# Kernel tuning notes

Hardware: AMD Instinct MI355X
Metric: run time of the kernel (lower is better)

The kernel has to match this reference:

```python
import jax, jax.numpy as jnp
import numpy as np

B, H, S, D = 4, 16, 4096, 64

def setup_inputs() -> dict:
    key = jax.random.key(0)
    k1, k2, k3 = jax.random.split(key, 3)
    Q = jax.random.normal(k1, (B, H, S, D), dtype=jnp.float32)
    K = jax.random.normal(k2, (B, H, S, D), dtype=jnp.float32)
    V = jax.random.normal(k3, (B, H, S, D), dtype=jnp.float32)
    mask = jnp.ones((B, H, S), dtype=jnp.float32)
    return {"Q": Q, "K": K, "V": V, "mask": mask}

def reference(Q, K, V, mask):
    # elu(x)+1 feature map
    Qf = jax.nn.elu(Q) + 1.0
    Kf = (jax.nn.elu(K) + 1.0) * mask[..., None]
    # KV: [B,H,D,D] = sum_s K[s]^T V[s]
    KV = jnp.einsum('bhsd,bhse->bhde', Kf, V)
    # normalization: Z = 1 / (Q . sum_s K[s])  -> [B,H,S,1]
    Ksum = jnp.sum(Kf, axis=-2)  # [B,H,D]
    Z = 1.0 / jnp.einsum('bhsd,bhd->bhs', Qf, Ksum)[..., None]
    out = jnp.einsum('bhsd,bhde->bhse', Qf, KV) * Z
    return out
```

## Files before the change

### kernel.cpp

```cpp
#include <hip/hip_runtime.h>

#define S_LEN 4096
#define DIM 64
#define NHEAD 64
#define LDK 68
#define PHEAD 4160

__device__ __forceinline__ float elu1(float x) {
    return x > 0.0f ? x + 1.0f : __expf(x);
}

__global__ __launch_bounds__(256) void pass1_kv(
    const float* __restrict__ K, const float* __restrict__ V,
    const float* __restrict__ mask, float* __restrict__ partials, int sh)
{
    const int head  = blockIdx.x >> sh;
    const int chunk = blockIdx.x & ((1 << sh) - 1);
    const int ntile = (S_LEN / 64) >> sh;
    const int t  = threadIdx.x;
    const int tx = t & 15;
    const int ty = t >> 4;
    const int e0 = tx * 4;
    const int d0 = ty * 4;

    __shared__ float kf[64 * LDK];
    __shared__ float vf[64 * LDK];

    float acc[4][4] = {{0.f,0.f,0.f,0.f},{0.f,0.f,0.f,0.f},{0.f,0.f,0.f,0.f},{0.f,0.f,0.f,0.f}};
    float ks[4] = {0.f, 0.f, 0.f, 0.f};

    const long hbase = (long)head * S_LEN * DIM;

    for (int tile = 0; tile < ntile; ++tile) {
        const int sbase = (chunk * ntile + tile) * 64;
        __syncthreads();
        #pragma unroll
        for (int i = 0; i < 4; ++i) {
            const int v4  = i * 256 + t;
            const int row = v4 >> 4;
            const int col = (v4 & 15) * 4;
            const float4 kq = *(const float4*)(K + hbase + (long)(sbase + row) * DIM + col);
            const float4 vq = *(const float4*)(V + hbase + (long)(sbase + row) * DIM + col);
            const float m = mask[head * S_LEN + sbase + row];
            float4 ko;
            ko.x = elu1(kq.x) * m; ko.y = elu1(kq.y) * m;
            ko.z = elu1(kq.z) * m; ko.w = elu1(kq.w) * m;
            *(float4*)&kf[row * LDK + col] = ko;
            *(float4*)&vf[row * LDK + col] = vq;
        }
        __syncthreads();
        #pragma unroll 4
        for (int s = 0; s < 64; ++s) {
            const float4 kk = *(const float4*)&kf[s * LDK + d0];
            const float4 vv = *(const float4*)&vf[s * LDK + e0];
            acc[0][0] += kk.x * vv.x; acc[0][1] += kk.x * vv.y; acc[0][2] += kk.x * vv.z; acc[0][3] += kk.x * vv.w;
            acc[1][0] += kk.y * vv.x; acc[1][1] += kk.y * vv.y; acc[1][2] += kk.y * vv.z; acc[1][3] += kk.y * vv.w;
            acc[2][0] += kk.z * vv.x; acc[2][1] += kk.z * vv.y; acc[2][2] += kk.z * vv.z; acc[2][3] += kk.z * vv.w;
            acc[3][0] += kk.w * vv.x; acc[3][1] += kk.w * vv.y; acc[3][2] += kk.w * vv.z; acc[3][3] += kk.w * vv.w;
            ks[0] += kk.x; ks[1] += kk.y; ks[2] += kk.z; ks[3] += kk.w;
        }
    }

    float* P = partials + (long)((head << sh) + chunk) * PHEAD;
    #pragma unroll
    for (int ei = 0; ei < 4; ++ei) {
        float4 w = make_float4(acc[0][ei], acc[1][ei], acc[2][ei], acc[3][ei]);
        *(float4*)(P + (e0 + ei) * 64 + d0) = w;
    }
    if (tx == 0) {
        *(float4*)(P + 64 * 64 + d0) = make_float4(ks[0], ks[1], ks[2], ks[3]);
    }
}

__global__ __launch_bounds__(256) void reduce_kv(
    const float* __restrict__ partials, float* __restrict__ kvf, int nchunk)
{
    const int head  = blockIdx.x >> 3;
    const int slice = blockIdx.x & 7;
    const int lo = slice * (PHEAD / 8);
    const int hi = lo + (PHEAD / 8);
    for (int idx = lo + threadIdx.x; idx < hi; idx += 256) {
        float s = 0.f;
        for (int c = 0; c < nchunk; ++c)
            s += partials[((long)head * nchunk + c) * PHEAD + idx];
        kvf[(long)head * PHEAD + idx] = s;
    }
}

__global__ __launch_bounds__(256) void pass2_out(
    const float* __restrict__ Q, const float* __restrict__ kvf,
    float* __restrict__ out)
{
    const int head = blockIdx.x >> 4;
    const int tile = blockIdx.x & 15;
    const int t    = threadIdx.x;
    const int lane = t & 63;
    const int wave = t >> 6;
    const int lx   = lane & 15;

    __shared__ float sm[4][64 * 64];
    float* sl = sm[wave];

    const long hbase = (long)head * S_LEN * DIM;
    const int  rbase = tile * 256 + wave * 64;

    #pragma unroll
    for (int i = 0; i < 16; ++i) {
        const int row = i * 4 + (lane >> 4);
        const int g   = lane & 15;
        const float4 qv = *(const float4*)(Q + hbase + (long)(rbase + row) * DIM + g * 4);
        float4 qo;
        qo.x = elu1(qv.x); qo.y = elu1(qv.y); qo.z = elu1(qv.z); qo.w = elu1(qv.w);
        *(float4*)&sl[row * 64 + ((g ^ (row & 15)) * 4)] = qo;
    }
    __builtin_amdgcn_wave_barrier();

    float q[64];
    #pragma unroll
    for (int g = 0; g < 16; ++g) {
        const float4 v = *(const float4*)&sl[lane * 64 + ((g ^ lx) * 4)];
        q[g * 4 + 0] = v.x; q[g * 4 + 1] = v.y; q[g * 4 + 2] = v.z; q[g * 4 + 3] = v.w;
    }
    __builtin_amdgcn_wave_barrier();

    const float* __restrict__ kvt = kvf + (long)head * PHEAD;

    float denom = 0.f;
    #pragma unroll
    for (int d = 0; d < 64; ++d) denom += q[d] * kvt[64 * 64 + d];
    const float rz = 1.0f / denom;

    #pragma unroll 1
    for (int eg = 0; eg < 16; ++eg) {
        const float* __restrict__ r = kvt + eg * 256;
        float a[4];
        #pragma unroll
        for (int er = 0; er < 4; ++er) {
            float acc = 0.f;
            #pragma unroll
            for (int d = 0; d < 64; ++d) acc += q[d] * r[er * 64 + d];
            a[er] = acc;
        }
        *(float4*)&sl[lane * 64 + ((eg ^ lx) * 4)] =
            make_float4(a[0] * rz, a[1] * rz, a[2] * rz, a[3] * rz);
    }
    __builtin_amdgcn_wave_barrier();

    #pragma unroll
    for (int i = 0; i < 16; ++i) {
        const int row = i * 4 + (lane >> 4);
        const int g   = lane & 15;
        const float4 o = *(const float4*)&sl[row * 64 + ((g ^ (row & 15)) * 4)];
        *(float4*)(out + hbase + (long)(rbase + row) * DIM + g * 4) = o;
    }
}

extern "C" void kernel_launch(void* const* d_in, const int* in_sizes, int n_in,
                              void* d_out, int out_size, void* d_ws, size_t ws_size,
                              hipStream_t stream) {
    const float* Q    = (const float*)d_in[0];
    const float* K    = (const float*)d_in[1];
    const float* V    = (const float*)d_in[2];
    const float* mask = (const float*)d_in[3];
    float* out = (float*)d_out;

    const size_t need16 = ((size_t)NHEAD * 16 * PHEAD + (size_t)NHEAD * PHEAD) * sizeof(float);
    const int sh = (ws_size >= need16) ? 4 : 3;
    const int nchunk = 1 << sh;

    float* partials = (float*)d_ws;
    float* kvf = partials + (size_t)NHEAD * nchunk * PHEAD;

    pass1_kv<<<NHEAD * nchunk, 256, 0, stream>>>(K, V, mask, partials, sh);
    reduce_kv<<<NHEAD * 8, 256, 0, stream>>>(partials, kvf, nchunk);
    pass2_out<<<NHEAD * 16, 256, 0, stream>>>(Q, kvf, out);
}
```

Measured before the change: 326.6 us.

## Restructure KV pass to per-wave 8x8 tiles with register prefetch; halve pass2 LDS

pass1_kv now gives each wave its own contiguous row range with wave-private double-buffered LDS tiles. Each thread accumulates an 8x8 outer-product block, and the next tile is prefetched into registers, so block-wide barriers drop out of the main loop. The four waves' partial KV results are then reduced serially through LDS before the write-out. pass2_out processes the 64-wide rows in two halves with a 36-stride rotated LDS staging buffer, shrinking shared memory per block, and both kernels gain an occupancy hint of 4 in their launch bounds. The larger accumulator tile raises register pressure, and the serial 4-wave LDS reduction adds extra barriers.

Measured after the change: 315.4 us. 3.4% less time.

```diff
diff --git a/kernel.cpp b/kernel.cpp
--- a/kernel.cpp
+++ b/kernel.cpp
@@ -3,73 +3,131 @@
 #define S_LEN 4096
 #define DIM 64
 #define NHEAD 64
-#define LDK 68
 #define PHEAD 4160
+#define LDR 68
 
 __device__ __forceinline__ float elu1(float x) {
     return x > 0.0f ? x + 1.0f : __expf(x);
 }
 
-__global__ __launch_bounds__(256) void pass1_kv(
+__global__ __launch_bounds__(256, 4) void pass1_kv(
     const float* __restrict__ K, const float* __restrict__ V,
     const float* __restrict__ mask, float* __restrict__ partials, int sh)
 {
-    const int head  = blockIdx.x >> sh;
-    const int chunk = blockIdx.x & ((1 << sh) - 1);
-    const int ntile = (S_LEN / 64) >> sh;
-    const int t  = threadIdx.x;
-    const int tx = t & 15;
-    const int ty = t >> 4;
-    const int e0 = tx * 4;
-    const int d0 = ty * 4;
-
-    __shared__ float kf[64 * LDK];
-    __shared__ float vf[64 * LDK];
-
-    float acc[4][4] = {{0.f,0.f,0.f,0.f},{0.f,0.f,0.f,0.f},{0.f,0.f,0.f,0.f},{0.f,0.f,0.f,0.f}};
-    float ks[4] = {0.f, 0.f, 0.f, 0.f};
+    const int head = blockIdx.x >> sh;
+    const int blkc = blockIdx.x & ((1 << sh) - 1);
+    const int t    = threadIdx.x;
+    const int lane = t & 63;
+    const int wave = t >> 6;
+    const int ex   = lane & 7;
+    const int dy   = lane >> 3;
+    const int e0   = ex * 8;
+    const int d0   = dy * 8;
+
+    const int rows_per_wave = (S_LEN >> sh) >> 2;
+    const int ntiles = rows_per_wave >> 3;
+    const int srow0  = (blkc * 4 + wave) * rows_per_wave;
+
+    __shared__ float sm[4][2][2][8 * LDR];
 
     const long hbase = (long)head * S_LEN * DIM;
 
-    for (int tile = 0; tile < ntile; ++tile) {
-        const int sbase = (chunk * ntile + tile) * 64;
+    float acc[8][8];
+    #pragma unroll
+    for (int i = 0; i < 8; ++i)
+        #pragma unroll
+        for (int j = 0; j < 8; ++j) acc[i][j] = 0.f;
+    float ks[8] = {0.f,0.f,0.f,0.f,0.f,0.f,0.f,0.f};
+
+    float4 kr[2], vr[2];
+    float  mr[2];
+    auto load_tile = [&](int tile) {
+        const int srow = srow0 + tile * 8;
+        #pragma unroll
+        for (int j = 0; j < 2; ++j) {
+            const int v4   = j * 64 + lane;
+            const int row  = v4 >> 4;
+            const int colg = (v4 & 15) * 4;
+            kr[j] = *(const float4*)(K + hbase + (long)(srow + row) * DIM + colg);
+            vr[j] = *(const float4*)(V + hbase + (long)(srow + row) * DIM + colg);
+            mr[j] = mask[head * S_LEN + srow + row];
+        }
+    };
+
+    load_tile(0);
+    for (int tile = 0; tile < ntiles; ++tile) {
+        float* kf = sm[wave][tile & 1][0];
+        float* vf = sm[wave][tile & 1][1];
+        #pragma unroll
+        for (int j = 0; j < 2; ++j) {
+            const int v4   = j * 64 + lane;
+            const int row  = v4 >> 4;
+            const int colg = (v4 & 15) * 4;
+            float4 ko;
+            ko.x = elu1(kr[j].x) * mr[j]; ko.y = elu1(kr[j].y) * mr[j];
+            ko.z = elu1(kr[j].z) * mr[j]; ko.w = elu1(kr[j].w) * mr[j];
+            *(float4*)&kf[row * LDR + colg] = ko;
+            *(float4*)&vf[row * LDR + colg] = vr[j];
+        }
+        if (tile + 1 < ntiles) load_tile(tile + 1);
+        __builtin_amdgcn_wave_barrier();
+        #pragma unroll 2
+        for (int s = 0; s < 8; ++s) {
+            float kk[8], vv[8];
+            *(float4*)&kk[0] = *(const float4*)&kf[s * LDR + d0];
+            *(float4*)&kk[4] = *(const float4*)&kf[s * LDR + d0 + 4];
+            *(float4*)&vv[0] = *(const float4*)&vf[s * LDR + e0];
+            *(float4*)&vv[4] = *(const float4*)&vf[s * LDR + e0 + 4];
+            #pragma unroll
+            for (int ei = 0; ei < 8; ++ei)
+                #pragma unroll
+                for (int di = 0; di < 8; ++di)
+                    acc[ei][di] += kk[di] * vv[ei];
+            #pragma unroll
+            for (int di = 0; di < 8; ++di) ks[di] += kk[di];
+        }
+        __builtin_amdgcn_wave_barrier();
+    }
+
+    __syncthreads();
+    float* red = (float*)sm;
+    for (int w = 0; w < 4; ++w) {
+        if (wave == w) {
+            if (w == 0) {
+                #pragma unroll
+                for (int ei = 0; ei < 8; ++ei) {
+                    *(float4*)&red[(e0 + ei) * 64 + d0]     = make_float4(acc[ei][0], acc[ei][1], acc[ei][2], acc[ei][3]);
+                    *(float4*)&red[(e0 + ei) * 64 + d0 + 4] = make_float4(acc[ei][4], acc[ei][5], acc[ei][6], acc[ei][7]);
+                }
+                if (ex == 0) {
+                    *(float4*)&red[4096 + d0]     = make_float4(ks[0], ks[1], ks[2], ks[3]);
+                    *(float4*)&red[4096 + d0 + 4] = make_float4(ks[4], ks[5], ks[6], ks[7]);
+                }
+            } else {
+                #pragma unroll
+                for (int ei = 0; ei < 8; ++ei) {
+                    float4 a = *(float4*)&red[(e0 + ei) * 64 + d0];
+                    a.x += acc[ei][0]; a.y += acc[ei][1]; a.z += acc[ei][2]; a.w += acc[ei][3];
+                    *(float4*)&red[(e0 + ei) * 64 + d0] = a;
+                    float4 b = *(float4*)&red[(e0 + ei) * 64 + d0 + 4];
+                    b.x += acc[ei][4]; b.y += acc[ei][5]; b.z += acc[ei][6]; b.w += acc[ei][7];
+                    *(float4*)&red[(e0 + ei) * 64 + d0 + 4] = b;
+                }
+                if (ex == 0) {
+                    float4 a = *(float4*)&red[4096 + d0];
+                    a.x += ks[0]; a.y += ks[1]; a.z += ks[2]; a.w += ks[3];
+                    *(float4*)&red[4096 + d0] = a;
+                    float4 b = *(float4*)&red[4096 + d0 + 4];
+                    b.x += ks[4]; b.y += ks[5]; b.z += ks[6]; b.w += ks[7];
+                    *(float4*)&red[4096 + d0 + 4] = b;
+                }
+            }
+        }
         __syncthreads();
-        #pragma unroll
-        for (int i = 0; i < 4; ++i) {
-            const int v4  = i * 256 + t;
-            const int row = v4 >> 4;
-            const int col = (v4 & 15) * 4;
-            const float4 kq = *(const float4*)(K + hbase + (long)(sbase + row) * DIM + col);
-            const float4 vq = *(const float4*)(V + hbase + (long)(sbase + row) * DIM + col);
-            const float m = mask[head * S_LEN + sbase + row];
-            float4 ko;
-            ko.x = elu1(kq.x) * m; ko.y = elu1(kq.y) * m;
-            ko.z = elu1(kq.z) * m; ko.w = elu1(kq.w) * m;
-            *(float4*)&kf[row * LDK + col] = ko;
-            *(float4*)&vf[row * LDK + col] = vq;
-        }
-        __syncthreads();
-        #pragma unroll 4
-        for (int s = 0; s < 64; ++s) {
-            const float4 kk = *(const float4*)&kf[s * LDK + d0];
-            const float4 vv = *(const float4*)&vf[s * LDK + e0];
-            acc[0][0] += kk.x * vv.x; acc[0][1] += kk.x * vv.y; acc[0][2] += kk.x * vv.z; acc[0][3] += kk.x * vv.w;
-            acc[1][0] += kk.y * vv.x; acc[1][1] += kk.y * vv.y; acc[1][2] += kk.y * vv.z; acc[1][3] += kk.y * vv.w;
-            acc[2][0] += kk.z * vv.x; acc[2][1] += kk.z * vv.y; acc[2][2] += kk.z * vv.z; acc[2][3] += kk.z * vv.w;
-            acc[3][0] += kk.w * vv.x; acc[3][1] += kk.w * vv.y; acc[3][2] += kk.w * vv.z; acc[3][3] += kk.w * vv.w;
-            ks[0] += kk.x; ks[1] += kk.y; ks[2] += kk.z; ks[3] += kk.w;
-        }
-    }
-
-    float* P = partials + (long)((head << sh) + chunk) * PHEAD;
-    #pragma unroll
-    for (int ei = 0; ei < 4; ++ei) {
-        float4 w = make_float4(acc[0][ei], acc[1][ei], acc[2][ei], acc[3][ei]);
-        *(float4*)(P + (e0 + ei) * 64 + d0) = w;
-    }
-    if (tx == 0) {
-        *(float4*)(P + 64 * 64 + d0) = make_float4(ks[0], ks[1], ks[2], ks[3]);
-    }
+    }
+    float* P = partials + (long)((head << sh) + blkc) * PHEAD;
+    for (int i = t; i < PHEAD / 4; i += 256)
+        *(float4*)(P + i * 4) = *(const float4*)&red[i * 4];
 }
 
 __global__ __launch_bounds__(256) void reduce_kv(
@@ -87,7 +145,7 @@
     }
 }
 
-__global__ __launch_bounds__(256) void pass2_out(
+__global__ __launch_bounds__(256, 4) void pass2_out(
     const float* __restrict__ Q, const float* __restrict__ kvf,
     float* __restrict__ out)
 {
@@ -96,32 +154,35 @@
     const int t    = threadIdx.x;
     const int lane = t & 63;
     const int wave = t >> 6;
-    const int lx   = lane & 15;
-
-    __shared__ float sm[4][64 * 64];
+
+    __shared__ float sm[4][64 * 36];
     float* sl = sm[wave];
 
     const long hbase = (long)head * S_LEN * DIM;
     const int  rbase = tile * 256 + wave * 64;
 
-    #pragma unroll
-    for (int i = 0; i < 16; ++i) {
-        const int row = i * 4 + (lane >> 4);
-        const int g   = lane & 15;
-        const float4 qv = *(const float4*)(Q + hbase + (long)(rbase + row) * DIM + g * 4);
-        float4 qo;
-        qo.x = elu1(qv.x); qo.y = elu1(qv.y); qo.z = elu1(qv.z); qo.w = elu1(qv.w);
-        *(float4*)&sl[row * 64 + ((g ^ (row & 15)) * 4)] = qo;
-    }
-    __builtin_amdgcn_wave_barrier();
-
     float q[64];
     #pragma unroll
-    for (int g = 0; g < 16; ++g) {
-        const float4 v = *(const float4*)&sl[lane * 64 + ((g ^ lx) * 4)];
-        q[g * 4 + 0] = v.x; q[g * 4 + 1] = v.y; q[g * 4 + 2] = v.z; q[g * 4 + 3] = v.w;
-    }
-    __builtin_amdgcn_wave_barrier();
+    for (int h = 0; h < 2; ++h) {
+        #pragma unroll
+        for (int i = 0; i < 8; ++i) {
+            const int v4  = i * 64 + lane;
+            const int row = v4 >> 3;
+            const int g   = v4 & 7;
+            const float4 qv = *(const float4*)(Q + hbase + (long)(rbase + row) * DIM + h * 32 + g * 4);
+            float4 qo;
+            qo.x = elu1(qv.x); qo.y = elu1(qv.y); qo.z = elu1(qv.z); qo.w = elu1(qv.w);
+            *(float4*)&sl[row * 36 + ((g + row) & 7) * 4] = qo;
+        }
+        __builtin_amdgcn_wave_barrier();
+        #pragma unroll
+        for (int g = 0; g < 8; ++g) {
+            const float4 v = *(const float4*)&sl[lane * 36 + ((g + lane) & 7) * 4];
+            q[h * 32 + g * 4 + 0] = v.x; q[h * 32 + g * 4 + 1] = v.y;
+            q[h * 32 + g * 4 + 2] = v.z; q[h * 32 + g * 4 + 3] = v.w;
+        }
+        __builtin_amdgcn_wave_barrier();
+    }
 
     const float* __restrict__ kvt = kvf + (long)head * PHEAD;
 
@@ -130,28 +191,32 @@
     for (int d = 0; d < 64; ++d) denom += q[d] * kvt[64 * 64 + d];
     const float rz = 1.0f / denom;
 
-    #pragma unroll 1
-    for (int eg = 0; eg < 16; ++eg) {
-        const float* __restrict__ r = kvt + eg * 256;
-        float a[4];
-        #pragma unroll
-        for (int er = 0; er < 4; ++er) {
-            float acc = 0.f;
+    #pragma unroll
+    for (int h = 0; h < 2; ++h) {
+        #pragma unroll 1
+        for (int eg = 0; eg < 8; ++eg) {
+            const float* __restrict__ r = kvt + (h * 8 + eg) * 256;
+            float a[4];
             #pragma unroll
-            for (int d = 0; d < 64; ++d) acc += q[d] * r[er * 64 + d];
-            a[er] = acc;
-        }
-        *(float4*)&sl[lane * 64 + ((eg ^ lx) * 4)] =
-            make_float4(a[0] * rz, a[1] * rz, a[2] * rz, a[3] * rz);
-    }
-    __builtin_amdgcn_wave_barrier();
-
-    #pragma unroll
-    for (int i = 0; i < 16; ++i) {
-        const int row = i * 4 + (lane >> 4);
-        const int g   = lane & 15;
-        const float4 o = *(const float4*)&sl[row * 64 + ((g ^ (row & 15)) * 4)];
-        *(float4*)(out + hbase + (long)(rbase + row) * DIM + g * 4) = o;
+            for (int er = 0; er < 4; ++er) {
+                float s = 0.f;
+                #pragma unroll
+                for (int d = 0; d < 64; ++d) s += q[d] * r[er * 64 + d];
+                a[er] = s;
+            }
+            *(float4*)&sl[lane * 36 + ((eg + lane) & 7) * 4] =
+                make_float4(a[0] * rz, a[1] * rz, a[2] * rz, a[3] * rz);
+        }
+        __builtin_amdgcn_wave_barrier();
+        #pragma unroll
+        for (int i = 0; i < 8; ++i) {
+            const int v4  = i * 64 + lane;
+            const int row = v4 >> 3;
+            const int g   = v4 & 7;
+            const float4 o = *(const float4*)&sl[row * 36 + ((g + row) & 7) * 4];
+            *(float4*)(out + hbase + (long)(rbase + row) * DIM + h * 32 + g * 4) = o;
+        }
+        __builtin_amdgcn_wave_barrier();
     }
 }
 
```
